# Optimization experiments

Measured on AMD Instinct MI355X. Metric: run time of the kernel, lower is better.

The kernel has to match this reference:

```python
import jax, jax.numpy as jnp
import numpy as np

N_WIRES = 16
N_LAYERS = 6
BATCH = 128


def setup_inputs() -> dict:
    key = jax.random.key(0)
    k1, k2 = jax.random.split(key)
    # embedding angles in [-pi, pi]
    x = jax.random.uniform(k1, (BATCH, N_WIRES), jnp.float32, -np.pi, np.pi)
    # StronglyEntanglingLayers weights, as in __init__: 0.2 * normal
    w = 0.2 * jax.random.normal(k2, (N_LAYERS, N_WIRES, 3), jnp.float32)
    return {"x": x, "w": w}


def _apply_1q(psi, U, wire, n):
    # psi: (B, 2^n) complex; U: (2,2) or (B,2,2) complex. Wire 0 = most significant bit.
    B = psi.shape[0]
    psi = psi.reshape(B, 2 ** wire, 2, -1)
    if U.ndim == 2:
        out = jnp.einsum('ab,nlbr->nlar', U, psi)
    else:
        out = jnp.einsum('nab,nlbr->nlar', U, psi)
    return out.reshape(B, -1)


def _apply_cnot(psi, c, t, n):
    # CNOT with control c, target t: flip target axis on the control=1 subspace.
    B = psi.shape[0]
    psi = psi.reshape((B,) + (2,) * n)
    ac, at = c + 1, t + 1  # tensor axes (axis 0 is batch)
    a0 = jnp.take(psi, 0, axis=ac)
    a1 = jnp.take(psi, 1, axis=ac)
    t_ax = at - 1 if at > ac else at  # target axis after removing control axis
    a1 = jnp.flip(a1, axis=t_ax)
    psi = jnp.stack([a0, a1], axis=ac)
    return psi.reshape(B, -1)


def _rot_matrix(phi, theta, omega):
    # PennyLane Rot(phi, theta, omega) = RZ(omega) RY(theta) RZ(phi)
    c, s = jnp.cos(theta / 2), jnp.sin(theta / 2)
    m00 = jnp.exp(-0.5j * (phi + omega)) * c
    m01 = -jnp.exp(0.5j * (phi - omega)) * s
    m10 = jnp.exp(-0.5j * (phi - omega)) * s
    m11 = jnp.exp(0.5j * (phi + omega)) * c
    return jnp.stack([jnp.stack([m00, m01]), jnp.stack([m10, m11])]).astype(jnp.complex64)


def _circuit(x, w):
    B, n = x.shape
    n_layers = w.shape[0]
    psi = jnp.zeros((B, 2 ** n), jnp.complex64).at[:, 0].set(1.0)

    # AngleEmbedding, rotation='Y': RY(x_i) on wire i (batched 2x2, real entries)
    c, s = jnp.cos(x / 2), jnp.sin(x / 2)  # (B, n)
    for i in range(n):
        U = jnp.stack([jnp.stack([c[:, i], -s[:, i]], -1),
                       jnp.stack([s[:, i], c[:, i]], -1)], -2).astype(jnp.complex64)
        psi = _apply_1q(psi, U, i, n)

    # StronglyEntanglingLayers: per layer, Rot on every wire then ring of CNOTs
    for l in range(n_layers):
        for i in range(n):
            U = _rot_matrix(w[l, i, 0], w[l, i, 1], w[l, i, 2])
            psi = _apply_1q(psi, U, i, n)
        r = (l % (n - 1)) + 1 if n > 1 else 0  # default PennyLane ranges
        if r:
            for i in range(n):
                psi = _apply_cnot(psi, i, (i + r) % n, n)

    # <Z_i> = P(bit_i = 0) - P(bit_i = 1)
    probs = psi.real ** 2 + psi.imag ** 2  # (B, 2^n)
    p = probs.reshape((B,) + (2,) * n)
    z = []
    for i in range(n):
        axes = tuple(a for a in range(1, n + 1) if a != i + 1)
        m = p.sum(axis=axes)  # (B, 2)
        z.append(m[:, 0] - m[:, 1])
    return jnp.stack(z, axis=-1).astype(jnp.float32)  # (B, n_wires)


def reference(x, w):
    return _circuit(x, w)
```

## Files before the change

### kernel.cpp

```cpp
#include <hip/hip_runtime.h>
#include <utility>


#define NW    16
#define P1BLK 1024
#define P2BLK 512
#define CHUNK 8192
#define LDSN  (CHUNK + CHUNK / 16)

template<class F, int... Is>
__device__ __forceinline__ void static_for_impl(F&& f, std::integer_sequence<int, Is...>) {
    (f(std::integral_constant<int, Is>{}), ...);
}
template<int N, class F>
__device__ __forceinline__ void static_for(F&& f) {
    static_for_impl(f, std::make_integer_sequence<int, N>{});
}

__device__ __forceinline__ int pidx(int u) { return u + (u >> 4); }

__device__ __forceinline__ void c2x2(float2& a0, float2& a1,
                                     float2 m00, float2 m01,
                                     float2 m10, float2 m11) {
    float2 r0, r1;
    r0.x = m00.x*a0.x - m00.y*a0.y + m01.x*a1.x - m01.y*a1.y;
    r0.y = m00.x*a0.y + m00.y*a0.x + m01.x*a1.y + m01.y*a1.x;
    r1.x = m10.x*a0.x - m10.y*a0.y + m11.x*a1.x - m11.y*a1.y;
    r1.y = m10.x*a0.y + m10.y*a0.x + m11.x*a1.y + m11.y*a1.x;
    a0 = r0; a1 = r1;
}

__device__ __forceinline__ float2 cmul(float2 a, float2 b) {
    return make_float2(a.x*b.x - a.y*b.y, a.x*b.y + a.y*b.x);
}

template<int Q>
__device__ __forceinline__ void rot_regs(float2 a[16], float2 m00, float2 m01,
                                         float2 m10, float2 m11) {
#pragma unroll
    for (int j = 0; j < 16; ++j)
        if (!((j >> Q) & 1))
            c2x2(a[j], a[j | (1 << Q)], m00, m01, m10, m11);
}

template<int QC, int QT>
__device__ __forceinline__ void cnot_inreg(float2 a[16]) {
#pragma unroll
    for (int j = 0; j < 16; ++j)
        if (((j >> QC) & 1) && !((j >> QT) & 1)) {
            float2 t = a[j]; a[j] = a[j | (1 << QT)]; a[j | (1 << QT)] = t;
        }
}

template<int QT>
__device__ __forceinline__ void cnot_ctrlout(float2 a[16], int ctrl) {
#pragma unroll
    for (int j = 0; j < 16; ++j)
        if (!((j >> QT) & 1)) {
            int j2 = j | (1 << QT);
            float2 x = a[j], y = a[j2];
            a[j].x  = ctrl ? y.x : x.x;  a[j].y  = ctrl ? y.y : x.y;
            a[j2].x = ctrl ? x.x : y.x;  a[j2].y = ctrl ? x.y : y.y;
        }
}

__device__ __forceinline__ void rot_mat(const float* ww, float2 m[4]) {
    float phi = ww[0], th = ww[1], om = ww[2];
    float ct, st;   sincosf(0.5f * th, &st, &ct);
    float cap, sap; sincosf(0.5f * (phi + om), &sap, &cap);
    float cam, sam; sincosf(0.5f * (phi - om), &sam, &cam);
    m[0] = make_float2( cap * ct, -sap * ct);
    m[1] = make_float2(-cam * st, -sam * st);
    m[2] = make_float2( cam * st, -sam * st);
    m[3] = make_float2( cap * ct,  sap * ct);
}

constexpr int swof(int tb) { return tb >= 9 ? 1 : tb >= 5 ? 2 : tb >= 1 ? 3 : 4; }

template<int L, int S>
__device__ __forceinline__ int sweep_gates(float2 a[16], const float2 (*gm)[4],
                                           int ub, int c) {
    constexpr int r    = L + 1;
    constexpr int base = (S == 1) ? 9 : (S == 2) ? 5 : (S == 3) ? 1 : 0;
    constexpr int rlo  = base;
    constexpr int rhi  = (S == 1) ? 12 : (S == 2) ? 8 : (S == 3) ? 4 : 0;
    static_for<rhi - rlo + 1>([&](auto K) {
        constexpr int bb   = rhi - decltype(K)::value;
        constexpr int wire = 15 - bb;
        rot_regs<bb - base>(a, gm[wire][0], gm[wire][1], gm[wire][2], gm[wire][3]);
    });
    int wmask = 0;
    static_for<16>([&](auto I) {
        constexpr int i = decltype(I)::value;
        if constexpr (i + r < 16) {
            constexpr int cb = 15 - i, tb = cb - r;
            constexpr bool skip = (L == 0 && i <= 1) || (L == 1 && i == 0);
            if constexpr (!skip && swof(tb) == S) {
                if constexpr (cb >= base && cb <= base + 3) {
                    cnot_inreg<cb - base, tb - base>(a);
                } else {
                    int ctrl = (cb >= 13) ? ((c >> (cb - 13)) & 1)
                                          : ((ub >> cb) & 1);
                    constexpr int ts = tb - r;
                    if constexpr (ts >= 0 && swof(ts) == S)
                        cnot_ctrlout<tb - base>(a, ctrl);
                    else
                        wmask |= ctrl << (tb - base);
                }
            }
        }
    });
    return wmask;
}

template<int LL>
__global__ __launch_bounds__(P1BLK)
void k_p1(const float* __restrict__ w, float2* __restrict__ psi) {
    const int b = blockIdx.x >> 2;
    const int T = ((blockIdx.x & 3) << 10) | (int)threadIdx.x;
    float2* g = psi + ((size_t)b << 16);
    const int sb = T << 1;

    float2 m0[4], m1[4], m2[4];
    rot_mat(w + (LL * NW + 0) * 3, m0);
    rot_mat(w + (LL * NW + 1) * 3, m1);
    rot_mat(w + (LL * NW + 2) * 3, m2);

    float2 a[16];
#pragma unroll
    for (int jh = 0; jh < 8; ++jh) {
        int s = sb | ((jh & 1) << 13) | (((jh >> 1) & 1) << 14) | (((jh >> 2) & 1) << 15);
        float4 f = *reinterpret_cast<const float4*>(g + s);
        a[(jh << 1)]     = make_float2(f.x, f.y);
        a[(jh << 1) | 1] = make_float2(f.z, f.w);
    }

    if constexpr (LL == 1) {
        cnot_inreg<0, 3>(a);
    } else if constexpr (LL == 2) {
        cnot_ctrlout<3>(a, (sb >> 1) & 1);
        cnot_inreg<0, 2>(a);
    } else if constexpr (LL == 3) {
        cnot_ctrlout<3>(a, (sb >> 2) & 1);
        cnot_ctrlout<2>(a, (sb >> 1) & 1);
        cnot_inreg<0, 1>(a);
    } else if constexpr (LL == 4) {
        cnot_ctrlout<3>(a, (sb >> 3) & 1);
        cnot_ctrlout<2>(a, (sb >> 2) & 1);
        cnot_ctrlout<1>(a, (sb >> 1) & 1);
    } else {
        cnot_ctrlout<3>(a, (sb >> 4) & 1);
        cnot_ctrlout<2>(a, (sb >> 3) & 1);
        cnot_ctrlout<1>(a, (sb >> 2) & 1);
    }

    rot_regs<3>(a, m0[0], m0[1], m0[2], m0[3]);
    rot_regs<2>(a, m1[0], m1[1], m1[2], m1[3]);
    rot_regs<1>(a, m2[0], m2[1], m2[2], m2[3]);
    if constexpr (LL == 1) cnot_inreg<3, 1>(a);

#pragma unroll
    for (int jh = 0; jh < 8; ++jh) {
        int s = sb | ((jh & 1) << 13) | (((jh >> 1) & 1) << 14) | (((jh >> 2) & 1) << 15);
        float2 lo = a[(jh << 1)], hi = a[(jh << 1) | 1];
        *reinterpret_cast<float4*>(g + s) = make_float4(lo.x, lo.y, hi.x, hi.y);
    }
}

template<int L>
__global__ __launch_bounds__(P2BLK, 4)
void k_p2(const float* __restrict__ x, const float* __restrict__ w,
          float* __restrict__ out, float2* __restrict__ psi) {
    __shared__ float2 lds[LDSN];
    __shared__ float2 gm[NW][4];
    __shared__ float  ecs[NW], ess[NW], accs[NW];
    const int b = blockIdx.x >> 3, c = blockIdx.x & 7;
    const int tid = threadIdx.x;
    float2* g = psi + ((size_t)b << 16) + ((size_t)c << 13);

    if (tid < NW) {
        rot_mat(w + (L * NW + tid) * 3, gm[tid]);
        if (L == 0) {
            float s_, c_; sincosf(0.5f * x[b * NW + tid], &s_, &c_);
            ecs[tid] = c_; ess[tid] = s_;
        }
        if (L == 5) accs[tid] = 0.f;
    }
    __syncthreads();

    float2 a[16];
    {
        const int ub = tid;
        if constexpr (L == 0) {
            float2 v[3][2];
#pragma unroll
            for (int wq = 0; wq < 3; ++wq)
#pragma unroll
                for (int bb = 0; bb < 2; ++bb) {
                    v[wq][bb].x = gm[wq][2*bb].x * ecs[wq] + gm[wq][2*bb+1].x * ess[wq];
                    v[wq][bb].y = gm[wq][2*bb].y * ecs[wq] + gm[wq][2*bb+1].y * ess[wq];
                }
            const int c2 = (c >> 2) & 1, c1 = (c >> 1) & 1, c0 = c & 1;
            float2 cs = cmul(cmul(v[0][c2], v[1][c1 ^ c2]), v[2][c0 ^ c1]);
            float plo = 1.0f;
#pragma unroll
            for (int k = 0; k < 9; ++k)
                plo *= ((tid >> k) & 1) ? ess[15 - k] : ecs[15 - k];
#pragma unroll
            for (int j = 0; j < 16; ++j) {
                float f = plo * ((j & 8) ? ess[3] : ecs[3])
                              * ((j & 4) ? ess[4] : ecs[4])
                              * ((j & 2) ? ess[5] : ecs[5])
                              * ((j & 1) ? ess[6] : ecs[6]);
                a[j] = make_float2(cs.x * f, cs.y * f);
            }
        } else {
#pragma unroll
            for (int j = 0; j < 16; ++j)
                a[j] = g[tid | (j << 9)];
        }
        int wm = sweep_gates<L, 1>(a, gm, ub, c) << 9;
#pragma unroll
        for (int j = 0; j < 16; ++j) lds[pidx((tid | (j << 9)) ^ wm)] = a[j];
    }
    __syncthreads();
    {
        const int ub = (tid & 31) | ((tid >> 5) << 9);
#pragma unroll
        for (int j = 0; j < 16; ++j) a[j] = lds[pidx(ub | (j << 5))];
        int wm = sweep_gates<L, 2>(a, gm, ub, c) << 5;
#pragma unroll
        for (int j = 0; j < 16; ++j) lds[pidx((ub | (j << 5)) ^ wm)] = a[j];
    }
    __syncthreads();
    {
        const int ub = (tid & 1) | ((tid >> 1) << 5);
#pragma unroll
        for (int j = 0; j < 16; ++j) a[j] = lds[pidx(ub | (j << 1))];
        int wm = sweep_gates<L, 3>(a, gm, ub, c) << 1;
#pragma unroll
        for (int j = 0; j < 16; ++j) lds[pidx((ub | (j << 1)) ^ wm)] = a[j];
    }
    __syncthreads();
    {
        const int ub = tid << 4;
#pragma unroll
        for (int j = 0; j < 16; ++j) a[j] = lds[pidx(ub | j)];
        int wm = sweep_gates<L, 4>(a, gm, ub, c);

        if constexpr (L == 5) {
            float psum = 0.f, sb3 = 0.f, sb2 = 0.f, sb1 = 0.f, sb0 = 0.f;
#pragma unroll
            for (int j = 0; j < 16; ++j) {
                int jj = j ^ wm;
                float2 v2 = a[j];
                float p = v2.x * v2.x + v2.y * v2.y;
                psum += p;
                sb3 += (jj & 8) ? -p : p;
                sb2 += (jj & 4) ? -p : p;
                sb1 += (jj & 2) ? -p : p;
                sb0 += (jj & 1) ? -p : p;
            }
            const int c2 = (c >> 2) & 1, c1 = (c >> 1) & 1, c0 = c & 1;
            float z[NW];
            z[0]  = ((c2 ^ (tid >> 1)) & 1) ? -psum : psum;
            z[1]  = ((c1 ^ tid) & 1)        ? -psum : psum;
            z[2]  = c0 ? -sb3 : sb3;
            z[3]  = ((tid >> 8) & 1) ? -sb2 : sb2;
            z[4]  = ((tid >> 7) & 1) ? -sb1 : sb1;
            z[5]  = ((tid >> 6) & 1) ? -sb0 : sb0;
#pragma unroll
            for (int i = 6; i < 12; ++i)
                z[i] = ((tid >> (11 - i)) & 1) ? -psum : psum;
            z[12] = sb3; z[13] = sb2; z[14] = sb1; z[15] = sb0;
#pragma unroll
            for (int i = 0; i < NW; ++i) {
                float v2 = z[i];
#pragma unroll
                for (int off = 32; off > 0; off >>= 1)
                    v2 += __shfl_down(v2, off, 64);
                if ((tid & 63) == 0) atomicAdd(&accs[i], v2);
            }
            __syncthreads();
            if (tid < NW) atomicAdd(&out[b * NW + tid], accs[tid]);
        } else {
#pragma unroll
            for (int j = 0; j < 16; ++j) lds[pidx((ub | j) ^ wm)] = a[j];
            __syncthreads();
#pragma unroll
            for (int it = 0; it < CHUNK / 2 / P2BLK; ++it) {
                int v = tid + it * P2BLK;
                int u = 2 * v;
                int wm0 = 0, wm1 = 0;
                static_for<(L >= 3) ? (L - 2) : 0>([&](auto K) {
                    constexpr int k  = decltype(K)::value;
                    constexpr int cbb = L - 3 - k, tbb = 12 - k;
                    wm0 |= ((u >> cbb) & 1) << tbb;
                    wm1 |= (((u | 1) >> cbb) & 1) << tbb;
                });
                float2 lo = lds[pidx(u ^ wm0)];
                float2 hi = lds[pidx((u | 1) ^ wm1)];
                reinterpret_cast<float4*>(g)[v] = make_float4(lo.x, lo.y, hi.x, hi.y);
            }
        }
    }
}

extern "C" void kernel_launch(void* const* d_in, const int* in_sizes, int n_in,
                              void* d_out, int out_size, void* d_ws, size_t ws_size,
                              hipStream_t stream) {
    const float* x = (const float*)d_in[0];
    const float* w = (const float*)d_in[1];
    float* out = (float*)d_out;
    float2* psi = (float2*)d_ws;

    const int batch = in_sizes[0] / NW;
    const int g1 = batch * 4;
    const int g2 = batch * 8;

    hipMemsetAsync(d_out, 0, (size_t)out_size * sizeof(float), stream);

    k_p2<0><<<g2, P2BLK, 0, stream>>>(x, w, out, psi);
    k_p1<1><<<g1, P1BLK, 0, stream>>>(w, psi);
    k_p2<1><<<g2, P2BLK, 0, stream>>>(x, w, out, psi);
    k_p1<2><<<g1, P1BLK, 0, stream>>>(w, psi);
    k_p2<2><<<g2, P2BLK, 0, stream>>>(x, w, out, psi);
    k_p1<3><<<g1, P1BLK, 0, stream>>>(w, psi);
    k_p2<3><<<g2, P2BLK, 0, stream>>>(x, w, out, psi);
    k_p1<4><<<g1, P1BLK, 0, stream>>>(w, psi);
    k_p2<4><<<g2, P2BLK, 0, stream>>>(x, w, out, psi);
    k_p1<5><<<g1, P1BLK, 0, stream>>>(w, psi);
    k_p2<5><<<g2, P2BLK, 0, stream>>>(x, w, out, psi);
}
```

Baseline: 493.6 us.

## Fold CNOT rings into index permutations and generate first layer analytically

The per-layer CNOT ring is now treated as a linear bit permutation (sigma_cx) applied during the LDS-to-global writeback, instead of executing CNOTs inside the sweeps. This removes the in-register swaps and the masked LDS scatter. The first layer's state is computed in closed form in a new k_gen kernel, which writes the product state after layer-0 rotations and CNOTs via Gray-code indexing. The final layer computes expectations with parity signs derived from the permuted indices. Wire 15's rotation moves into k_p1, and the mid sweeps become plain rotations. The cost is subtle index algebra that must match the reference CNOT ordering exactly.

```diff
diff --git a/kernel.cpp b/kernel.cpp
--- a/kernel.cpp
+++ b/kernel.cpp
@@ -75,42 +75,77 @@
     m[3] = make_float2( cap * ct,  sap * ct);
 }
 
-constexpr int swof(int tb) { return tb >= 9 ? 1 : tb >= 5 ? 2 : tb >= 1 ? 3 : 4; }
-
-template<int L, int S>
-__device__ __forceinline__ int sweep_gates(float2 a[16], const float2 (*gm)[4],
-                                           int ub, int c) {
-    constexpr int r    = L + 1;
-    constexpr int base = (S == 1) ? 9 : (S == 2) ? 5 : (S == 3) ? 1 : 0;
-    constexpr int rlo  = base;
-    constexpr int rhi  = (S == 1) ? 12 : (S == 2) ? 8 : (S == 3) ? 4 : 0;
-    static_for<rhi - rlo + 1>([&](auto K) {
-        constexpr int bb   = rhi - decltype(K)::value;
-        constexpr int wire = 15 - bb;
-        rot_regs<bb - base>(a, gm[wire][0], gm[wire][1], gm[wire][2], gm[wire][3]);
-    });
-    int wmask = 0;
-    static_for<16>([&](auto I) {
-        constexpr int i = decltype(I)::value;
-        if constexpr (i + r < 16) {
-            constexpr int cb = 15 - i, tb = cb - r;
-            constexpr bool skip = (L == 0 && i <= 1) || (L == 1 && i == 0);
-            if constexpr (!skip && swof(tb) == S) {
-                if constexpr (cb >= base && cb <= base + 3) {
-                    cnot_inreg<cb - base, tb - base>(a);
-                } else {
-                    int ctrl = (cb >= 13) ? ((c >> (cb - 13)) & 1)
-                                          : ((ub >> cb) & 1);
-                    constexpr int ts = tb - r;
-                    if constexpr (ts >= 0 && swof(ts) == S)
-                        cnot_ctrlout<tb - base>(a, ctrl);
-                    else
-                        wmask |= ctrl << (tb - base);
-                }
-            }
+#define SSTEP(cb, tb) s ^= ((s >> (cb)) & 1) << (tb);
+template<int L>
+constexpr int sigma_cx(int s) {
+    if constexpr (L == 1) {
+        SSTEP(2,0) SSTEP(3,1) SSTEP(4,2) SSTEP(5,3) SSTEP(6,4) SSTEP(7,5)
+        SSTEP(8,6) SSTEP(9,7) SSTEP(10,8) SSTEP(11,9) SSTEP(12,10)
+        SSTEP(13,11) SSTEP(14,12)
+    } else if constexpr (L == 2) {
+        SSTEP(3,0) SSTEP(4,1) SSTEP(5,2) SSTEP(6,3) SSTEP(7,4) SSTEP(8,5)
+        SSTEP(9,6) SSTEP(10,7) SSTEP(11,8) SSTEP(12,9) SSTEP(13,10)
+        SSTEP(14,11) SSTEP(15,12)
+    } else if constexpr (L == 3) {
+        SSTEP(0,12)
+        SSTEP(4,0) SSTEP(5,1) SSTEP(6,2) SSTEP(7,3) SSTEP(8,4) SSTEP(9,5)
+        SSTEP(10,6) SSTEP(11,7) SSTEP(12,8) SSTEP(13,9) SSTEP(14,10)
+        SSTEP(15,11)
+    } else if constexpr (L == 4) {
+        SSTEP(0,11) SSTEP(1,12)
+        SSTEP(5,0) SSTEP(6,1) SSTEP(7,2) SSTEP(8,3) SSTEP(9,4) SSTEP(10,5)
+        SSTEP(11,6) SSTEP(12,7) SSTEP(13,8) SSTEP(14,9) SSTEP(15,10)
+    }
+    return s;
+}
+#undef SSTEP
+
+__global__ __launch_bounds__(P2BLK)
+void k_gen(const float* __restrict__ x, const float* __restrict__ w,
+           float2* __restrict__ psi) {
+    __shared__ float2 gm[NW][4];
+    __shared__ float  ecs[NW], ess[NW];
+    const int b = blockIdx.x >> 3, c = blockIdx.x & 7;
+    const int tid = threadIdx.x;
+    float2* g = psi + ((size_t)b << 16) + ((size_t)c << 13);
+
+    if (tid < NW) {
+        rot_mat(w + tid * 3, gm[tid]);
+        float s_, c_; sincosf(0.5f * x[b * NW + tid], &s_, &c_);
+        ecs[tid] = c_; ess[tid] = s_;
+    }
+    __syncthreads();
+
+    auto fsel = [&](int wq, int bit) {
+        float2 glo = gm[wq][2*bit], ghi = gm[wq][2*bit+1];
+        return make_float2(glo.x * ecs[wq] + ghi.x * ess[wq],
+                           glo.y * ecs[wq] + ghi.y * ess[wq]);
+    };
+
+    const int U0 = (c << 13) | (tid << 4);
+    const int S0 = U0 ^ (U0 >> 1);
+
+    float2 common = fsel(0, (S0 >> 15) & 1);
+#pragma unroll
+    for (int wq = 1; wq < 12; ++wq)
+        common = cmul(common, fsel(wq, (S0 >> (15 - wq)) & 1));
+
+#pragma unroll
+    for (int j = 0; j < 16; j += 2) {
+        float2 amp2[2];
+#pragma unroll
+        for (int k = 0; k < 2; ++k) {
+            int U = U0 | (j + k);
+            int S = U ^ (U >> 1);
+            float2 t = cmul(common, fsel(12, (S >> 3) & 1));
+            t = cmul(t, fsel(13, (S >> 2) & 1));
+            t = cmul(t, fsel(14, (S >> 1) & 1));
+            t = cmul(t, fsel(15, S & 1));
+            amp2[k] = t;
         }
-    });
-    return wmask;
+        reinterpret_cast<float4*>(g)[(tid << 3) | (j >> 1)] =
+            make_float4(amp2[0].x, amp2[0].y, amp2[1].x, amp2[1].y);
+    }
 }
 
 template<int LL>
@@ -121,10 +156,11 @@
     float2* g = psi + ((size_t)b << 16);
     const int sb = T << 1;
 
-    float2 m0[4], m1[4], m2[4];
+    float2 m0[4], m1[4], m2[4], m15[4];
     rot_mat(w + (LL * NW + 0) * 3, m0);
     rot_mat(w + (LL * NW + 1) * 3, m1);
     rot_mat(w + (LL * NW + 2) * 3, m2);
+    rot_mat(w + (LL * NW + 15) * 3, m15);
 
     float2 a[16];
 #pragma unroll
@@ -154,9 +190,10 @@
         cnot_ctrlout<1>(a, (sb >> 2) & 1);
     }
 
-    rot_regs<3>(a, m0[0], m0[1], m0[2], m0[3]);
-    rot_regs<2>(a, m1[0], m1[1], m1[2], m1[3]);
-    rot_regs<1>(a, m2[0], m2[1], m2[2], m2[3]);
+    rot_regs<3>(a, m0[0],  m0[1],  m0[2],  m0[3]);
+    rot_regs<2>(a, m1[0],  m1[1],  m1[2],  m1[3]);
+    rot_regs<1>(a, m2[0],  m2[1],  m2[2],  m2[3]);
+    rot_regs<0>(a, m15[0], m15[1], m15[2], m15[3]);
     if constexpr (LL == 1) cnot_inreg<3, 1>(a);
 
 #pragma unroll
@@ -168,142 +205,137 @@
 }
 
 template<int L>
+__device__ __forceinline__ void sweeps123(float2 (*gm)[4], float2* lds,
+                                          float2 a[16], int tid,
+                                          const float2* __restrict__ g) {
+    rot_regs<3>(a, gm[3][0], gm[3][1], gm[3][2], gm[3][3]);
+    rot_regs<2>(a, gm[4][0], gm[4][1], gm[4][2], gm[4][3]);
+    rot_regs<1>(a, gm[5][0], gm[5][1], gm[5][2], gm[5][3]);
+    rot_regs<0>(a, gm[6][0], gm[6][1], gm[6][2], gm[6][3]);
+#pragma unroll
+    for (int j = 0; j < 16; ++j) lds[pidx(tid | (j << 9))] = a[j];
+    __syncthreads();
+    {
+        const int ub = (tid & 31) | ((tid >> 5) << 9);
+#pragma unroll
+        for (int j = 0; j < 16; ++j) a[j] = lds[pidx(ub | (j << 5))];
+        rot_regs<3>(a, gm[7][0],  gm[7][1],  gm[7][2],  gm[7][3]);
+        rot_regs<2>(a, gm[8][0],  gm[8][1],  gm[8][2],  gm[8][3]);
+        rot_regs<1>(a, gm[9][0],  gm[9][1],  gm[9][2],  gm[9][3]);
+        rot_regs<0>(a, gm[10][0], gm[10][1], gm[10][2], gm[10][3]);
+#pragma unroll
+        for (int j = 0; j < 16; ++j) lds[pidx(ub | (j << 5))] = a[j];
+    }
+    __syncthreads();
+    {
+        const int ub = (tid & 1) | ((tid >> 1) << 5);
+#pragma unroll
+        for (int j = 0; j < 16; ++j) a[j] = lds[pidx(ub | (j << 1))];
+        rot_regs<3>(a, gm[11][0], gm[11][1], gm[11][2], gm[11][3]);
+        rot_regs<2>(a, gm[12][0], gm[12][1], gm[12][2], gm[12][3]);
+        rot_regs<1>(a, gm[13][0], gm[13][1], gm[13][2], gm[13][3]);
+        rot_regs<0>(a, gm[14][0], gm[14][1], gm[14][2], gm[14][3]);
+    }
+}
+
+template<int L>
 __global__ __launch_bounds__(P2BLK, 4)
-void k_p2(const float* __restrict__ x, const float* __restrict__ w,
-          float* __restrict__ out, float2* __restrict__ psi) {
+void k_mid(const float* __restrict__ w, float2* __restrict__ psi) {
     __shared__ float2 lds[LDSN];
     __shared__ float2 gm[NW][4];
-    __shared__ float  ecs[NW], ess[NW], accs[NW];
     const int b = blockIdx.x >> 3, c = blockIdx.x & 7;
     const int tid = threadIdx.x;
     float2* g = psi + ((size_t)b << 16) + ((size_t)c << 13);
 
-    if (tid < NW) {
-        rot_mat(w + (L * NW + tid) * 3, gm[tid]);
-        if (L == 0) {
-            float s_, c_; sincosf(0.5f * x[b * NW + tid], &s_, &c_);
-            ecs[tid] = c_; ess[tid] = s_;
-        }
-        if (L == 5) accs[tid] = 0.f;
-    }
-    __syncthreads();
-
+    if (tid < NW) rot_mat(w + (L * NW + tid) * 3, gm[tid]);
     float2 a[16];
-    {
-        const int ub = tid;
-        if constexpr (L == 0) {
-            float2 v[3][2];
-#pragma unroll
-            for (int wq = 0; wq < 3; ++wq)
-#pragma unroll
-                for (int bb = 0; bb < 2; ++bb) {
-                    v[wq][bb].x = gm[wq][2*bb].x * ecs[wq] + gm[wq][2*bb+1].x * ess[wq];
-                    v[wq][bb].y = gm[wq][2*bb].y * ecs[wq] + gm[wq][2*bb+1].y * ess[wq];
-                }
-            const int c2 = (c >> 2) & 1, c1 = (c >> 1) & 1, c0 = c & 1;
-            float2 cs = cmul(cmul(v[0][c2], v[1][c1 ^ c2]), v[2][c0 ^ c1]);
-            float plo = 1.0f;
-#pragma unroll
-            for (int k = 0; k < 9; ++k)
-                plo *= ((tid >> k) & 1) ? ess[15 - k] : ecs[15 - k];
-#pragma unroll
-            for (int j = 0; j < 16; ++j) {
-                float f = plo * ((j & 8) ? ess[3] : ecs[3])
-                              * ((j & 4) ? ess[4] : ecs[4])
-                              * ((j & 2) ? ess[5] : ecs[5])
-                              * ((j & 1) ? ess[6] : ecs[6]);
-                a[j] = make_float2(cs.x * f, cs.y * f);
-            }
-        } else {
-#pragma unroll
-            for (int j = 0; j < 16; ++j)
-                a[j] = g[tid | (j << 9)];
-        }
-        int wm = sweep_gates<L, 1>(a, gm, ub, c) << 9;
-#pragma unroll
-        for (int j = 0; j < 16; ++j) lds[pidx((tid | (j << 9)) ^ wm)] = a[j];
-    }
-    __syncthreads();
-    {
-        const int ub = (tid & 31) | ((tid >> 5) << 9);
-#pragma unroll
-        for (int j = 0; j < 16; ++j) a[j] = lds[pidx(ub | (j << 5))];
-        int wm = sweep_gates<L, 2>(a, gm, ub, c) << 5;
-#pragma unroll
-        for (int j = 0; j < 16; ++j) lds[pidx((ub | (j << 5)) ^ wm)] = a[j];
-    }
-    __syncthreads();
+#pragma unroll
+    for (int j = 0; j < 16; ++j) a[j] = g[tid | (j << 9)];
+    __syncthreads();
+
+    sweeps123<L>(gm, lds, a, tid, g);
     {
         const int ub = (tid & 1) | ((tid >> 1) << 5);
 #pragma unroll
-        for (int j = 0; j < 16; ++j) a[j] = lds[pidx(ub | (j << 1))];
-        int wm = sweep_gates<L, 3>(a, gm, ub, c) << 1;
-#pragma unroll
-        for (int j = 0; j < 16; ++j) lds[pidx((ub | (j << 1)) ^ wm)] = a[j];
-    }
-    __syncthreads();
-    {
-        const int ub = tid << 4;
-#pragma unroll
-        for (int j = 0; j < 16; ++j) a[j] = lds[pidx(ub | j)];
-        int wm = sweep_gates<L, 4>(a, gm, ub, c);
-
-        if constexpr (L == 5) {
-            float psum = 0.f, sb3 = 0.f, sb2 = 0.f, sb1 = 0.f, sb0 = 0.f;
-#pragma unroll
-            for (int j = 0; j < 16; ++j) {
-                int jj = j ^ wm;
-                float2 v2 = a[j];
-                float p = v2.x * v2.x + v2.y * v2.y;
-                psum += p;
-                sb3 += (jj & 8) ? -p : p;
-                sb2 += (jj & 4) ? -p : p;
-                sb1 += (jj & 2) ? -p : p;
-                sb0 += (jj & 1) ? -p : p;
-            }
-            const int c2 = (c >> 2) & 1, c1 = (c >> 1) & 1, c0 = c & 1;
-            float z[NW];
-            z[0]  = ((c2 ^ (tid >> 1)) & 1) ? -psum : psum;
-            z[1]  = ((c1 ^ tid) & 1)        ? -psum : psum;
-            z[2]  = c0 ? -sb3 : sb3;
-            z[3]  = ((tid >> 8) & 1) ? -sb2 : sb2;
-            z[4]  = ((tid >> 7) & 1) ? -sb1 : sb1;
-            z[5]  = ((tid >> 6) & 1) ? -sb0 : sb0;
-#pragma unroll
-            for (int i = 6; i < 12; ++i)
-                z[i] = ((tid >> (11 - i)) & 1) ? -psum : psum;
-            z[12] = sb3; z[13] = sb2; z[14] = sb1; z[15] = sb0;
-#pragma unroll
-            for (int i = 0; i < NW; ++i) {
-                float v2 = z[i];
-#pragma unroll
-                for (int off = 32; off > 0; off >>= 1)
-                    v2 += __shfl_down(v2, off, 64);
-                if ((tid & 63) == 0) atomicAdd(&accs[i], v2);
-            }
-            __syncthreads();
-            if (tid < NW) atomicAdd(&out[b * NW + tid], accs[tid]);
-        } else {
-#pragma unroll
-            for (int j = 0; j < 16; ++j) lds[pidx((ub | j) ^ wm)] = a[j];
-            __syncthreads();
-#pragma unroll
-            for (int it = 0; it < CHUNK / 2 / P2BLK; ++it) {
-                int v = tid + it * P2BLK;
-                int u = 2 * v;
-                int wm0 = 0, wm1 = 0;
-                static_for<(L >= 3) ? (L - 2) : 0>([&](auto K) {
-                    constexpr int k  = decltype(K)::value;
-                    constexpr int cbb = L - 3 - k, tbb = 12 - k;
-                    wm0 |= ((u >> cbb) & 1) << tbb;
-                    wm1 |= (((u | 1) >> cbb) & 1) << tbb;
-                });
-                float2 lo = lds[pidx(u ^ wm0)];
-                float2 hi = lds[pidx((u | 1) ^ wm1)];
-                reinterpret_cast<float4*>(g)[v] = make_float4(lo.x, lo.y, hi.x, hi.y);
-            }
-        }
-    }
+        for (int j = 0; j < 16; ++j) lds[pidx(ub | (j << 1))] = a[j];
+    }
+    __syncthreads();
+
+    const int sbase = sigma_cx<L>((c << 13) | (tid << 1));
+    constexpr int D0 = sigma_cx<L>(1);
+    static_for<CHUNK / 2 / P2BLK>([&](auto ITC) {
+        constexpr int IT  = decltype(ITC)::value;
+        constexpr int KIT = sigma_cx<L>(IT << 10);
+        int ae = sbase ^ KIT;
+        float2 lo = lds[pidx(ae & 0x1FFF)];
+        float2 hi = lds[pidx((ae ^ D0) & 0x1FFF)];
+        reinterpret_cast<float4*>(g)[tid + IT * P2BLK] =
+            make_float4(lo.x, lo.y, hi.x, hi.y);
+    });
+}
+
+__global__ __launch_bounds__(P2BLK, 4)
+void k_last(const float* __restrict__ w, float* __restrict__ out,
+            float2* __restrict__ psi) {
+    __shared__ float2 lds[LDSN];
+    __shared__ float2 gm[NW][4];
+    __shared__ float  accs[NW];
+    const int b = blockIdx.x >> 3, c = blockIdx.x & 7;
+    const int tid = threadIdx.x;
+    float2* g = psi + ((size_t)b << 16) + ((size_t)c << 13);
+
+    if (tid < NW) { rot_mat(w + (5 * NW + tid) * 3, gm[tid]); accs[tid] = 0.f; }
+    float2 a[16];
+#pragma unroll
+    for (int j = 0; j < 16; ++j) a[j] = g[tid | (j << 9)];
+    __syncthreads();
+
+    sweeps123<5>(gm, lds, a, tid, g);
+
+    float psum = 0.f, sb3 = 0.f, sb2 = 0.f, sb1 = 0.f, sb0 = 0.f;
+#pragma unroll
+    for (int j = 0; j < 16; ++j) {
+        float2 v = a[j];
+        float p = v.x * v.x + v.y * v.y;
+        psum += p;
+        sb3 += (j & 8) ? -p : p;
+        sb2 += (j & 4) ? -p : p;
+        sb1 += (j & 2) ? -p : p;
+        sb0 += (j & 1) ? -p : p;
+    }
+    const int q  = tid & 1;
+    const int t1 = (tid >> 1) & 1, t2 = (tid >> 2) & 1, t3 = (tid >> 3) & 1;
+    const int t4 = (tid >> 4) & 1, t5 = (tid >> 5) & 1, t6 = (tid >> 6) & 1;
+    const int t7 = (tid >> 7) & 1, t8 = (tid >> 8) & 1;
+    const int c13 = c & 1, c14 = (c >> 1) & 1, c15 = (c >> 2) & 1;
+
+    float z[NW];
+    z[0]  = ((c15 ^ t7 ^ t1) & 1)       ? -psum : psum;
+    z[1]  = ((c14 ^ t6) & 1)            ? -sb3  : sb3;
+    z[2]  = ((c15 ^ c13 ^ t5) & 1)      ? -sb2  : sb2;
+    z[3]  = ((c14 ^ t8 ^ t4) & 1)       ? -sb1  : sb1;
+    z[4]  = ((c13 ^ t7 ^ t3) & 1)       ? -sb0  : sb0;
+    z[5]  = ((t8 ^ t6 ^ t2 ^ q) & 1)    ? -psum : psum;
+    z[6]  = ((c15 ^ t5) & 1)            ? -psum : psum;
+    z[7]  = ((c14 ^ t4) & 1)            ? -psum : psum;
+    z[8]  = ((c13 ^ t3) & 1)            ? -psum : psum;
+    z[9]  = ((t8 ^ t2) & 1)             ? -psum : psum;
+    z[10] = ((t7 ^ t1) & 1)             ? -psum : psum;
+    z[11] = (t6 & 1)                    ? -sb3  : sb3;
+    z[12] = ((c15 ^ t5) & 1)            ? -sb2  : sb2;
+    z[13] = ((c14 ^ t4) & 1)            ? -sb1  : sb1;
+    z[14] = ((c13 ^ t3) & 1)            ? -sb0  : sb0;
+    z[15] = ((t8 ^ t2 ^ q) & 1)         ? -psum : psum;
+
+#pragma unroll
+    for (int i = 0; i < NW; ++i) {
+        float v = z[i];
+#pragma unroll
+        for (int off = 32; off > 0; off >>= 1) v += __shfl_down(v, off, 64);
+        if ((tid & 63) == 0) atomicAdd(&accs[i], v);
+    }
+    __syncthreads();
+    if (tid < NW) atomicAdd(&out[b * NW + tid], accs[tid]);
 }
 
 extern "C" void kernel_launch(void* const* d_in, const int* in_sizes, int n_in,
@@ -320,15 +352,15 @@
 
     hipMemsetAsync(d_out, 0, (size_t)out_size * sizeof(float), stream);
 
-    k_p2<0><<<g2, P2BLK, 0, stream>>>(x, w, out, psi);
+    k_gen<<<g2, P2BLK, 0, stream>>>(x, w, psi);
     k_p1<1><<<g1, P1BLK, 0, stream>>>(w, psi);
-    k_p2<1><<<g2, P2BLK, 0, stream>>>(x, w, out, psi);
+    k_mid<1><<<g2, P2BLK, 0, stream>>>(w, psi);
     k_p1<2><<<g1, P1BLK, 0, stream>>>(w, psi);
-    k_p2<2><<<g2, P2BLK, 0, stream>>>(x, w, out, psi);
+    k_mid<2><<<g2, P2BLK, 0, stream>>>(w, psi);
     k_p1<3><<<g1, P1BLK, 0, stream>>>(w, psi);
-    k_p2<3><<<g2, P2BLK, 0, stream>>>(x, w, out, psi);
+    k_mid<3><<<g2, P2BLK, 0, stream>>>(w, psi);
     k_p1<4><<<g1, P1BLK, 0, stream>>>(w, psi);
-    k_p2<4><<<g2, P2BLK, 0, stream>>>(x, w, out, psi);
+    k_mid<4><<<g2, P2BLK, 0, stream>>>(w, psi);
     k_p1<5><<<g1, P1BLK, 0, stream>>>(w, psi);
-    k_p2<5><<<g2, P2BLK, 0, stream>>>(x, w, out, psi);
-}
+    k_last<<<g2, P2BLK, 0, stream>>>(w, out, psi);
+}
```

Measured after the change: 532.0 us. +7.8%, slower.
